# Performance work log

Measured on AMD Instinct MI355X. Metric: run time of the kernel, lower is better.

The kernel has to match this reference:

```python
import jax, jax.numpy as jnp
import numpy as np

B = 4096       # batch
D = 256        # num_features
H = 512        # proposal_hidden_units
K = 10         # mixture_components
C = 64         # context_units
L = 4          # proposal_residual_blocks
S = 10         # num_importance_samples (call default)
HEAD = 3 * K + C
LOG2PI = float(np.log(2.0 * np.pi))


def setup_inputs() -> dict:
    key = jax.random.key(0)
    ks = jax.random.split(key, 10)
    x = jax.random.normal(ks[0], (B, D), jnp.float32)
    observed_mask = (jax.random.uniform(ks[1], (B, D)) < 0.5).astype(jnp.float32)
    s_in = 1.0 / np.sqrt(2 * D)
    s_h = 1.0 / np.sqrt(H)
    W_in = (jax.random.normal(ks[2], (2 * D, H), jnp.float32) * s_in)
    b_in = jnp.zeros((H,), jnp.float32)
    W1 = jax.random.normal(ks[3], (L, H, H), jnp.float32) * s_h
    b1 = jnp.zeros((L, H), jnp.float32)
    W2 = jax.random.normal(ks[4], (L, H, H), jnp.float32) * s_h
    b2 = jnp.zeros((L, H), jnp.float32)
    W_fin = jax.random.normal(ks[5], (H, D * HEAD), jnp.float32) * s_h
    b_fin = jnp.zeros((D * HEAD,), jnp.float32)
    return {
        "x": x, "observed_mask": observed_mask,
        "W_in": W_in, "b_in": b_in,
        "W1": W1, "b1": b1, "W2": W2, "b2": b2,
        "W_fin": W_fin, "b_fin": b_fin,
        "num_importance_samples": S,
    }


def _proposal_params(x_o, observed_mask, W_in, b_in, W1, b1, W2, b2, W_fin, b_fin):
    # Residual MLP proposal network on [x_o, observed_mask].
    h = jnp.concatenate([x_o, observed_mask], axis=-1) @ W_in + b_in  # [B, H]
    for l in range(L):
        r = jax.nn.relu(h) @ W1[l] + b1[l]
        r = jax.nn.relu(r) @ W2[l] + b2[l]
        h = h + r
    out = (h @ W_fin + b_fin).reshape(h.shape[0], D, HEAD)  # [B, D, 3K+C]
    logits = out[..., :K]
    means = out[..., K:2 * K]
    scales = jax.nn.softplus(out[..., 2 * K:3 * K]) + 1e-3
    return logits, means, scales


def reference(x, observed_mask, W_in, b_in, W1, b1, W2, b2, W_fin, b_fin,
              num_importance_samples):
    query = 1.0 - observed_mask
    x_o = x * observed_mask
    x_u = x * query

    logits, means, scales = _proposal_params(
        x_o, observed_mask, W_in, b_in, W1, b1, W2, b2, W_fin, b_fin)

    # Per-feature mixture-of-Gaussians log-likelihood of x_u, masked by query.
    log_w = jax.nn.log_softmax(logits, axis=-1)               # [B, D, K]
    z = (x_u[..., None] - means) / scales
    comp_ll = -0.5 * z * z - jnp.log(scales) - 0.5 * LOG2PI   # [B, D, K]
    proposal_ll = jax.scipy.special.logsumexp(log_w + comp_ll, axis=-1) * query

    # Samples (stop_gradient in the original).
    skey = jax.random.key(1234)
    kc, kn = jax.random.split(skey)
    comp = jax.random.categorical(kc, logits, axis=-1,
                                  shape=(num_importance_samples,) + logits.shape[:2])  # [S, B, D]
    mu = jnp.take_along_axis(means[None], comp[..., None], axis=-1)[..., 0]    # [S, B, D]
    sg = jnp.take_along_axis(scales[None], comp[..., None], axis=-1)[..., 0]   # [S, B, D]
    eps = jax.random.normal(kn, comp.shape, jnp.float32)
    samples = mu + sg * eps                                   # [S, B, D]
    samples = jnp.transpose(samples, (1, 0, 2))               # [B, S, D]
    samples = jax.lax.stop_gradient(samples) * query[:, None, :]
    # call() multiplies by query twice (before and after selected_features block)
    proposal_samples = samples * query[:, None, :]

    proposal_mean = jnp.sum(jax.nn.softmax(logits, axis=-1) * means, axis=-1) * query
    proposal_mean = proposal_mean * query  # second masking, as in call()

    return proposal_ll, proposal_samples, proposal_mean
```

## Files before the change

### kernel.cpp

```cpp
#include <hip/hip_runtime.h>
#include <cstdint>

#define B 4096
#define D 256
#define H 512
#define K 10
#define NL 4
#define S 10
#define NOUT 30
#define HEADW 94
#define ND (B*D)
#define NLOG 2560
#define NMS  5120

typedef __bf16 bf16x8 __attribute__((ext_vector_type(8)));
typedef float  f32x16 __attribute__((ext_vector_type(16)));

__host__ __device__ inline void threefry2x32(uint32_t k0, uint32_t k1,
                                             uint32_t x0, uint32_t x1,
                                             uint32_t& o0, uint32_t& o1) {
  uint32_t ks2 = k0 ^ k1 ^ 0x1BD11BDAu;
#define TF_ROT(x, r) (((x) << (r)) | ((x) >> (32 - (r))))
#define TF_RND(r) { x0 += x1; x1 = TF_ROT(x1, r); x1 ^= x0; }
  x0 += k0; x1 += k1;
  TF_RND(13) TF_RND(15) TF_RND(26) TF_RND(6)
  x0 += k1; x1 += ks2 + 1u;
  TF_RND(17) TF_RND(29) TF_RND(16) TF_RND(24)
  x0 += ks2; x1 += k0 + 2u;
  TF_RND(13) TF_RND(15) TF_RND(26) TF_RND(6)
  x0 += k0; x1 += k1 + 3u;
  TF_RND(17) TF_RND(29) TF_RND(16) TF_RND(24)
  x0 += k1; x1 += ks2 + 4u;
  TF_RND(13) TF_RND(15) TF_RND(26) TF_RND(6)
  x0 += ks2; x1 += k0 + 5u;
  o0 = x0; o1 = x1;
#undef TF_RND
#undef TF_ROT
}

__device__ __forceinline__ uint32_t rb32(uint32_t k0, uint32_t k1, uint32_t idx) {
  uint32_t a, b;
  threefry2x32(k0, k1, 0u, idx, a, b);
  return a ^ b;
}

__device__ __forceinline__ float u01_from_bits(uint32_t bits) {
  return __uint_as_float((bits >> 9) | 0x3f800000u) - 1.0f;
}

__device__ __forceinline__ float erfinv_f32(float x) {
  float w = -log1pf(-x * x);
  float p;
  if (w < 5.0f) {
    w = w - 2.5f;
    p = 2.81022636e-08f;
    p = fmaf(p, w, 3.43273939e-07f);
    p = fmaf(p, w, -3.5233877e-06f);
    p = fmaf(p, w, -4.39150654e-06f);
    p = fmaf(p, w, 0.00021858087f);
    p = fmaf(p, w, -0.00125372503f);
    p = fmaf(p, w, -0.00417768164f);
    p = fmaf(p, w, 0.246640727f);
    p = fmaf(p, w, 1.50140941f);
  } else {
    w = sqrtf(w) - 3.0f;
    p = -0.000200214257f;
    p = fmaf(p, w, 0.000100950558f);
    p = fmaf(p, w, 0.00134934322f);
    p = fmaf(p, w, -0.00367342844f);
    p = fmaf(p, w, 0.00573950773f);
    p = fmaf(p, w, -0.0076224613f);
    p = fmaf(p, w, 0.00943887047f);
    p = fmaf(p, w, 1.00167406f);
    p = fmaf(p, w, 2.83297682f);
  }
  return p * x;
}

__device__ __forceinline__ unsigned short bf16_rne(float x) {
  uint32_t u = __float_as_uint(x);
  uint32_t r = u + 0x7fffu + ((u >> 16) & 1u);
  return (unsigned short)(r >> 16);
}

__device__ __forceinline__ void split2(float x, short& hi, short& lo) {
  unsigned short hb = bf16_rne(x);
  float hf = __uint_as_float((uint32_t)hb << 16);
  hi = (short)hb;
  lo = (short)bf16_rne(x - hf);
}

__device__ __forceinline__ void gload16(const void* g, void* l) {
  __builtin_amdgcn_global_load_lds(
      (const __attribute__((address_space(1))) void*)g,
      (__attribute__((address_space(3))) void*)l, 16, 0, 0);
}

template <int ROWS>
__device__ __forceinline__ void stage_region(const short* __restrict__ g,
                                             short* l, int wid, int lane) {
#pragma unroll
  for (int c = wid; c < ROWS / 16; c += 4) {
    const short* gp = g + (size_t)(c * 16 + (lane >> 2)) * 512 + (lane & 3) * 8;
    gload16(gp, l + c * 512);
  }
}

__global__ __launch_bounds__(256) void wgatherL(const float* __restrict__ Wf,
                                                float* __restrict__ wsgL) {
  int c = blockIdx.x * 256 + threadIdx.x;
  int k = blockIdx.y;
  int dd = c / K, j = c - dd * K;
  wsgL[(size_t)k * NLOG + c] = Wf[(size_t)k * (D * HEADW) + dd * HEADW + j];
}

__global__ __launch_bounds__(256) void wsplit_ms(const float* __restrict__ Wf,
                                                 short* __restrict__ whi,
                                                 short* __restrict__ wlo) {
  __shared__ float tile[32][33];
  int n0 = blockIdx.x * 32, k0 = blockIdx.y * 32;
  int tx = threadIdx.x & 31, ty = threadIdx.x >> 5;
#pragma unroll
  for (int r = 0; r < 4; ++r) {
    int k = k0 + ty + r * 8;
    int n = n0 + tx;
    int dd = n / 20, j = n - dd * 20;
    tile[ty + r * 8][tx] = Wf[(size_t)k * (D * HEADW) + dd * HEADW + 10 + j];
  }
  __syncthreads();
#pragma unroll
  for (int r = 0; r < 4; ++r) {
    int n = n0 + ty + r * 8;
    int k = k0 + tx;
    float v = tile[tx][ty + r * 8];
    short hb, lb;
    split2(v, hb, lb);
    whi[(size_t)n * 512 + k] = hb;
    wlo[(size_t)n * 512 + k] = lb;
  }
}

template <int RELU, int RES, int FP, int SPLIT>
__global__ __launch_bounds__(256) void gemm_trunk(const float* __restrict__ A,
                                                  const float* __restrict__ W,
                                                  const float* __restrict__ bias,
                                                  const float* res, float* C,
                                                  const float* __restrict__ xp,
                                                  const float* __restrict__ mp,
                                                  short* __restrict__ Ah,
                                                  short* __restrict__ Al) {
  __shared__ float As[64 * 68];
  __shared__ float Ws[64 * 64];
  const int tid = threadIdx.x;
  const int lane = tid & 63, wid = tid >> 6;
  const int tx = tid & 15, ty = tid >> 4;
  const int bm = blockIdx.y * 64, bn = blockIdx.x * 64;
  const int ls = tid & 15, lm = tid >> 4;

  float acc[4][4] = {};

  for (int k0 = 0; k0 < H; k0 += 64) {
#pragma unroll
    for (int c = wid; c < 16; c += 4) {
      gload16(W + (size_t)(k0 + c * 4 + (lane >> 4)) * H + bn + (lane & 15) * 4,
              Ws + c * 256 + lane * 4);
    }
#pragma unroll
    for (int r = 0; r < 4; ++r) {
      int m = lm + 16 * r;
      float4 f;
      if (FP) {
        int c = k0 + 4 * ls;
        const int brow = bm + m;
        if (c < D) {
          float4 xv = *(const float4*)(xp + (size_t)brow * D + c);
          float4 mv = *(const float4*)(mp + (size_t)brow * D + c);
          f.x = xv.x * mv.x; f.y = xv.y * mv.y;
          f.z = xv.z * mv.z; f.w = xv.w * mv.w;
        } else {
          f = *(const float4*)(mp + (size_t)brow * D + (c - D));
        }
      } else {
        f = *(const float4*)(A + (size_t)(bm + m) * H + k0 + 4 * ls);
      }
      if (RELU) {
        f.x = fmaxf(f.x, 0.0f); f.y = fmaxf(f.y, 0.0f);
        f.z = fmaxf(f.z, 0.0f); f.w = fmaxf(f.w, 0.0f);
      }
      As[(4 * ls + 0) * 68 + m] = f.x;
      As[(4 * ls + 1) * 68 + m] = f.y;
      As[(4 * ls + 2) * 68 + m] = f.z;
      As[(4 * ls + 3) * 68 + m] = f.w;
    }
    __syncthreads();
#pragma unroll
    for (int kk = 0; kk < 64; ++kk) {
      float4 a4 = *(const float4*)(As + kk * 68 + ty * 4);
      float4 b4 = *(const float4*)(Ws + kk * 64 + tx * 4);
      float a[4] = {a4.x, a4.y, a4.z, a4.w};
      float b[4] = {b4.x, b4.y, b4.z, b4.w};
#pragma unroll
      for (int i = 0; i < 4; ++i)
#pragma unroll
        for (int j = 0; j < 4; ++j) acc[i][j] = fmaf(a[i], b[j], acc[i][j]);
    }
    __syncthreads();
  }
#pragma unroll
  for (int i = 0; i < 4; ++i) {
    int row = bm + ty * 4 + i;
    float v[4];
#pragma unroll
    for (int j = 0; j < 4; ++j) {
      int col = bn + tx * 4 + j;
      v[j] = acc[i][j] + bias[col];
      if (RES) v[j] = res[(size_t)row * H + col] + v[j];
      C[(size_t)row * H + col] = v[j];
    }
    if (SPLIT) {
      short4 h4, l4;
      split2(v[0], h4.x, l4.x); split2(v[1], h4.y, l4.y);
      split2(v[2], h4.z, l4.z); split2(v[3], h4.w, l4.w);
      *(short4*)(Ah + (size_t)row * H + bn + tx * 4) = h4;
      *(short4*)(Al + (size_t)row * H + bn + tx * 4) = l4;
    }
  }
}

__global__ __launch_bounds__(256) void gemm_head(const float* __restrict__ A,
                                                 const float* __restrict__ Wg,
                                                 const short* __restrict__ Bh,
                                                 const short* __restrict__ Bl,
                                                 const short* __restrict__ Ah,
                                                 const short* __restrict__ Al,
                                                 const float* __restrict__ bf,
                                                 float* __restrict__ headL,
                                                 float* __restrict__ headMS) {
  __shared__ __align__(16) float smem[8448];
  const int tid = threadIdx.x;
  const int lane = tid & 63, wid = tid >> 6;
  const int bm = blockIdx.y * 128;

  if (blockIdx.x < 20) {
    float* As = smem;
    float* Ws = smem + 4352;
    const int tx = tid & 15, ty = tid >> 4;
    const int bn = blockIdx.x * 128;
    const int ls = tid & 7, lm = tid >> 3;

    float acc[8][8] = {};

    for (int k0 = 0; k0 < H; k0 += 32) {
#pragma unroll
      for (int c = wid; c < 16; c += 4) {
        gload16(Wg + (size_t)(k0 + c * 2 + (lane >> 5)) * NLOG + bn + (lane & 31) * 4,
                Ws + c * 256 + lane * 4);
      }
#pragma unroll
      for (int r = 0; r < 4; ++r) {
        int m = lm + 32 * r;
        float4 f = *(const float4*)(A + (size_t)(bm + m) * H + k0 + 4 * ls);
        As[(4 * ls + 0) * 136 + m] = f.x;
        As[(4 * ls + 1) * 136 + m] = f.y;
        As[(4 * ls + 2) * 136 + m] = f.z;
        As[(4 * ls + 3) * 136 + m] = f.w;
      }
      __syncthreads();
#pragma unroll
      for (int kk = 0; kk < 32; ++kk) {
        float a[8], b[8];
        *(float4*)(a + 0) = *(const float4*)(As + kk * 136 + ty * 8);
        *(float4*)(a + 4) = *(const float4*)(As + kk * 136 + ty * 8 + 4);
        *(float4*)(b + 0) = *(const float4*)(Ws + kk * 128 + tx * 8);
        *(float4*)(b + 4) = *(const float4*)(Ws + kk * 128 + tx * 8 + 4);
#pragma unroll
        for (int i = 0; i < 8; ++i)
#pragma unroll
          for (int j = 0; j < 8; ++j) acc[i][j] = fmaf(a[i], b[j], acc[i][j]);
      }
      __syncthreads();
    }
    float bias[8];
#pragma unroll
    for (int j = 0; j < 8; ++j) {
      int c = bn + tx * 8 + j;
      int dd = c / K, jj = c - dd * K;
      bias[j] = bf[dd * HEADW + jj];
    }
#pragma unroll
    for (int i = 0; i < 8; ++i) {
      int row = bm + ty * 8 + i;
      float4 v0, v1;
      v0.x = acc[i][0] + bias[0]; v0.y = acc[i][1] + bias[1];
      v0.z = acc[i][2] + bias[2]; v0.w = acc[i][3] + bias[3];
      v1.x = acc[i][4] + bias[4]; v1.y = acc[i][5] + bias[5];
      v1.z = acc[i][6] + bias[6]; v1.w = acc[i][7] + bias[7];
      float* dst = headL + (size_t)row * NLOG + bn + tx * 8;
      *(float4*)dst = v0;
      *(float4*)(dst + 4) = v1;
    }
  } else {
    short* lds = (short*)smem;
    const int wm = wid >> 1, wn = wid & 1;
    const int bn = (blockIdx.x - 20) * 128;

    short* ldsAh = lds;
    short* ldsAl = lds + 4096;
    short* ldsBh = lds + 8192;
    short* ldsBl = lds + 12288;

    const short* gBh = Bh + (size_t)bn * 512;
    const short* gBl = Bl + (size_t)bn * 512;
    const short* gAh = Ah + (size_t)bm * 512;
    const short* gAl = Al + (size_t)bm * 512;

    f32x16 acc[2][2];
#pragma unroll
    for (int mt = 0; mt < 2; ++mt)
#pragma unroll
      for (int nt = 0; nt < 2; ++nt)
#pragma unroll
        for (int i = 0; i < 16; ++i) acc[mt][nt][i] = 0.0f;

    for (int k0 = 0; k0 < 512; k0 += 32) {
      stage_region<128>(gBh + k0, ldsBh, wid, lane);
      stage_region<128>(gBl + k0, ldsBl, wid, lane);
      stage_region<128>(gAh + k0, ldsAh, wid, lane);
      stage_region<128>(gAl + k0, ldsAl, wid, lane);
      __syncthreads();
#pragma unroll
      for (int sub = 0; sub < 2; ++sub) {
        bf16x8 ah[2], al[2], bh[2], bl[2];
#pragma unroll
        for (int mt = 0; mt < 2; ++mt) {
          int r = wm * 64 + mt * 32 + (lane & 31);
          int off = r * 32 + sub * 16 + (lane >> 5) * 8;
          ah[mt] = *(const bf16x8*)(ldsAh + off);
          al[mt] = *(const bf16x8*)(ldsAl + off);
        }
#pragma unroll
        for (int nt = 0; nt < 2; ++nt) {
          int r = wn * 64 + nt * 32 + (lane & 31);
          int off = r * 32 + sub * 16 + (lane >> 5) * 8;
          bh[nt] = *(const bf16x8*)(ldsBh + off);
          bl[nt] = *(const bf16x8*)(ldsBl + off);
        }
#pragma unroll
        for (int mt = 0; mt < 2; ++mt)
#pragma unroll
          for (int nt = 0; nt < 2; ++nt) {
            acc[mt][nt] = __builtin_amdgcn_mfma_f32_32x32x16_bf16(ah[mt], bh[nt], acc[mt][nt], 0, 0, 0);
            acc[mt][nt] = __builtin_amdgcn_mfma_f32_32x32x16_bf16(ah[mt], bl[nt], acc[mt][nt], 0, 0, 0);
            acc[mt][nt] = __builtin_amdgcn_mfma_f32_32x32x16_bf16(al[mt], bh[nt], acc[mt][nt], 0, 0, 0);
          }
      }
      __syncthreads();
    }

#pragma unroll
    for (int mt = 0; mt < 2; ++mt)
#pragma unroll
      for (int nt = 0; nt < 2; ++nt) {
        int col = bn + wn * 64 + nt * 32 + (lane & 31);
        int rbase = bm + wm * 64 + mt * 32 + 4 * (lane >> 5);
        int dd = col / 20, j = col - dd * 20;
#pragma unroll
        for (int reg = 0; reg < 16; ++reg) {
          int row = rbase + (reg & 3) + 8 * (reg >> 2);
          float v = acc[mt][nt][reg] + bf[dd * HEADW + 10 + j];
          if (j >= 10) v = (fmaxf(v, 0.0f) + log1pf(expf(-fabsf(v)))) + 0.001f;
          headMS[(size_t)row * NMS + col] = v;
        }
      }
  }
}

__global__ __launch_bounds__(256) void compact_zero(const float* __restrict__ mask,
                                                    float* __restrict__ out_ll,
                                                    float* __restrict__ out_s,
                                                    float* __restrict__ out_mean,
                                                    int* __restrict__ list,
                                                    int* __restrict__ counter) {
  int idx = blockIdx.x * 256 + threadIdx.x;
  if (idx >= ND) return;
  if (mask[idx] != 0.0f) {
    int b = idx >> 8, d = idx & (D - 1);
    out_ll[idx] = 0.0f;
    out_mean[idx] = 0.0f;
#pragma unroll
    for (int s = 0; s < S; ++s) out_s[((size_t)b * S + s) * D + d] = 0.0f;
  } else {
    int pos = atomicAdd(counter, 1);
    list[pos] = idx;
  }
}

__global__ __launch_bounds__(256) void fused_tail(const float* __restrict__ headL,
                                                  const float* __restrict__ headMS,
                                                  const float* __restrict__ x,
                                                  const float* __restrict__ mask,
                                                  const int* __restrict__ list,
                                                  const int* __restrict__ counter,
                                                  float* __restrict__ out_ll,
                                                  float* __restrict__ out_s,
                                                  float* __restrict__ out_mean,
                                                  uint32_t kc0, uint32_t kc1,
                                                  uint32_t kn0, uint32_t kn1) {
  int i = blockIdx.x * 256 + threadIdx.x;
  if (i >= *counter) return;
  int idx = list[i];
  int b = idx >> 8, d = idx & (D - 1);
  const float* hpL = headL + (size_t)idx * K;
  const float* hpM = headMS + (size_t)idx * (2 * K);
  float lg[K], mn[K], sc[K];
#pragma unroll
  for (int k = 0; k < K; ++k) { lg[k] = hpL[k]; mn[k] = hpM[k]; sc[k] = hpM[K + k]; }
  float q = 1.0f - mask[idx];
  float xu = x[idx] * q;
  float m = lg[0];
#pragma unroll
  for (int k = 1; k < K; ++k) m = fmaxf(m, lg[k]);
  float e[K];
  float sum = 0.0f;
#pragma unroll
  for (int k = 0; k < K; ++k) { e[k] = expf(lg[k] - m); sum += e[k]; }
  float lse = logf(sum);
  float a[K];
  float amax = -3.402823466e38f;
#pragma unroll
  for (int k = 0; k < K; ++k) {
    float z = (xu - mn[k]) / sc[k];
    float cll = -0.5f * z * z - logf(sc[k]) - 0.9189385332046727f;
    float lw = (lg[k] - m) - lse;
    a[k] = lw + cll;
    amax = fmaxf(amax, a[k]);
  }
  float s2 = 0.0f;
#pragma unroll
  for (int k = 0; k < K; ++k) s2 += expf(a[k] - amax);
  out_ll[idx] = (logf(s2) + amax) * q;
  float pm = 0.0f;
#pragma unroll
  for (int k = 0; k < K; ++k) pm += (e[k] / sum) * mn[k];
  out_mean[idx] = pm * q;
  float inv_e[K];
#pragma unroll
  for (int k = 0; k < K; ++k) inv_e[k] = 1.0f / e[k];
  for (int s = 0; s < S; ++s) {
    uint32_t t32 = (uint32_t)s * (uint32_t)ND + (uint32_t)idx;
    uint32_t base = t32 * (uint32_t)K;
    int best = 0;
    float rbest = 3.402823466e38f;
#pragma unroll
    for (int k = 0; k < K; ++k) {
      uint32_t bits = rb32(kc0, kc1, base + (uint32_t)k);
      float u = u01_from_bits(bits);
      float wv = -__log2f(u);
      float r = wv * inv_e[k];
      if (r < rbest) { rbest = r; best = k; }
    }
    uint32_t ebits = rb32(kn0, kn1, t32);
    float f = u01_from_bits(ebits);
    float r2 = f * 2.0f + (-0.99999994f);
    r2 = fmaxf(r2, -0.99999994f);
    float eps = 1.4142135623730951f * erfinv_f32(r2);
    out_s[((size_t)b * S + s) * D + d] = (mn[best] + sc[best] * eps) * q;
  }
}

extern "C" void kernel_launch(void* const* d_in, const int* in_sizes, int n_in,
                              void* d_out, int out_size, void* d_ws, size_t ws_size,
                              hipStream_t stream) {
  const float* x    = (const float*)d_in[0];
  const float* mask = (const float*)d_in[1];
  const float* W_in = (const float*)d_in[2];
  const float* b_in = (const float*)d_in[3];
  const float* W1   = (const float*)d_in[4];
  const float* b1   = (const float*)d_in[5];
  const float* W2   = (const float*)d_in[6];
  const float* b2   = (const float*)d_in[7];
  const float* Wf   = (const float*)d_in[8];
  const float* bf   = (const float*)d_in[9];

  char* w = (char*)d_ws;
  float* headL  = (float*)w;
  float* headMS = (float*)(w + 41943040);
  float* t      = headL;
  float* h      = (float*)(w + 125829120);
  float* wsgL   = (float*)(w + 134217728);
  int*   list   = (int*)(w + 134217728);
  short* wms_h  = (short*)(w + 139460608);
  short* wms_l  = (short*)(w + 144703488);
  int*   counter = (int*)(w + 149946368);

  float* out_ll   = (float*)d_out;
  float* out_s    = out_ll + (size_t)ND;
  float* out_mean = out_s + (size_t)ND * S;

  short* Ah = (short*)out_s;
  short* Al = Ah + (size_t)B * H;

  wgatherL<<<dim3(NLOG / 256, 512), 256, 0, stream>>>(Wf, wsgL);
  wsplit_ms<<<dim3(NMS / 32, 512 / 32), 256, 0, stream>>>(Wf, wms_h, wms_l);

  dim3 gtr(H / 64, B / 64);
  gemm_trunk<0, 0, 1, 0><<<gtr, 256, 0, stream>>>(nullptr, W_in, b_in, nullptr,
                                                  h, x, mask, nullptr, nullptr);
  for (int l = 0; l < NL - 1; ++l) {
    gemm_trunk<1, 0, 0, 0><<<gtr, 256, 0, stream>>>(h, W1 + (size_t)l * H * H,
                                                    b1 + (size_t)l * H, nullptr,
                                                    t, nullptr, nullptr,
                                                    nullptr, nullptr);
    gemm_trunk<1, 1, 0, 0><<<gtr, 256, 0, stream>>>(t, W2 + (size_t)l * H * H,
                                                    b2 + (size_t)l * H, h, h,
                                                    nullptr, nullptr,
                                                    nullptr, nullptr);
  }
  gemm_trunk<1, 0, 0, 0><<<gtr, 256, 0, stream>>>(h, W1 + (size_t)3 * H * H,
                                                  b1 + (size_t)3 * H, nullptr,
                                                  t, nullptr, nullptr,
                                                  nullptr, nullptr);
  gemm_trunk<1, 1, 0, 1><<<gtr, 256, 0, stream>>>(t, W2 + (size_t)3 * H * H,
                                                  b2 + (size_t)3 * H, h, h,
                                                  nullptr, nullptr, Ah, Al);

  gemm_head<<<dim3(60, B / 128), 256, 0, stream>>>(h, wsgL, wms_h, wms_l,
                                                   Ah, Al, bf, headL, headMS);

  hipMemsetAsync(counter, 0, 4, stream);
  compact_zero<<<ND / 256, 256, 0, stream>>>(mask, out_ll, out_s, out_mean,
                                             list, counter);

  uint32_t kc0, kc1, kn0, kn1;
  threefry2x32(0u, 1234u, 0u, 0u, kc0, kc1);
  threefry2x32(0u, 1234u, 0u, 1u, kn0, kn1);
  fused_tail<<<ND / 256, 256, 0, stream>>>(headL, headMS, x, mask, list, counter,
                                           out_ll, out_s, out_mean,
                                           kc0, kc1, kn0, kn1);
}
```

Before: 1.130 ms.

## Fuse head weight gather and split kernels into first trunk GEMM launch

Removes the separate wgatherL and wsplit_ms launches. Their work now runs as extra blocks (blockIdx.x >= 8) inside the first trunk GEMM grid. The weight preprocessing overlaps with the input GEMM and two kernel launches go away. The grid grows to 128x64 blocks, and the extra blocks return early, which may change scheduling of the GEMM blocks.

After: 1.216 ms. 1.08x slower.

```diff
diff --git a/kernel.cpp b/kernel.cpp
--- a/kernel.cpp
+++ b/kernel.cpp
@@ -106,41 +106,7 @@
   }
 }
 
-__global__ __launch_bounds__(256) void wgatherL(const float* __restrict__ Wf,
-                                                float* __restrict__ wsgL) {
-  int c = blockIdx.x * 256 + threadIdx.x;
-  int k = blockIdx.y;
-  int dd = c / K, j = c - dd * K;
-  wsgL[(size_t)k * NLOG + c] = Wf[(size_t)k * (D * HEADW) + dd * HEADW + j];
-}
-
-__global__ __launch_bounds__(256) void wsplit_ms(const float* __restrict__ Wf,
-                                                 short* __restrict__ whi,
-                                                 short* __restrict__ wlo) {
-  __shared__ float tile[32][33];
-  int n0 = blockIdx.x * 32, k0 = blockIdx.y * 32;
-  int tx = threadIdx.x & 31, ty = threadIdx.x >> 5;
-#pragma unroll
-  for (int r = 0; r < 4; ++r) {
-    int k = k0 + ty + r * 8;
-    int n = n0 + tx;
-    int dd = n / 20, j = n - dd * 20;
-    tile[ty + r * 8][tx] = Wf[(size_t)k * (D * HEADW) + dd * HEADW + 10 + j];
-  }
-  __syncthreads();
-#pragma unroll
-  for (int r = 0; r < 4; ++r) {
-    int n = n0 + ty + r * 8;
-    int k = k0 + tx;
-    float v = tile[tx][ty + r * 8];
-    short hb, lb;
-    split2(v, hb, lb);
-    whi[(size_t)n * 512 + k] = hb;
-    wlo[(size_t)n * 512 + k] = lb;
-  }
-}
-
-template <int RELU, int RES, int FP, int SPLIT>
+template <int RELU, int RES, int FP, int SPLIT, int WP>
 __global__ __launch_bounds__(256) void gemm_trunk(const float* __restrict__ A,
                                                   const float* __restrict__ W,
                                                   const float* __restrict__ bias,
@@ -148,10 +114,49 @@
                                                   const float* __restrict__ xp,
                                                   const float* __restrict__ mp,
                                                   short* __restrict__ Ah,
-                                                  short* __restrict__ Al) {
+                                                  short* __restrict__ Al,
+                                                  const float* __restrict__ Wf,
+                                                  float* __restrict__ wsgL,
+                                                  short* __restrict__ whi,
+                                                  short* __restrict__ wlo) {
   __shared__ float As[64 * 68];
   __shared__ float Ws[64 * 64];
   const int tid = threadIdx.x;
+
+  if (WP && blockIdx.x >= 8) {
+    const int id = (blockIdx.x - 8) * 64 + blockIdx.y;
+    if (id < 5120) {
+      int c = (id % 10) * 256 + tid;
+      int k = id / 10;
+      int dd = c / K, j = c - dd * K;
+      wsgL[(size_t)k * NLOG + c] = Wf[(size_t)k * (D * HEADW) + dd * HEADW + j];
+    } else {
+      float (*tile)[33] = (float(*)[33])As;
+      int b2 = id - 5120;
+      int n0 = (b2 % 160) * 32, k0 = (b2 / 160) * 32;
+      int tx = tid & 31, ty = tid >> 5;
+#pragma unroll
+      for (int r = 0; r < 4; ++r) {
+        int k = k0 + ty + r * 8;
+        int n = n0 + tx;
+        int dd = n / 20, j = n - dd * 20;
+        tile[ty + r * 8][tx] = Wf[(size_t)k * (D * HEADW) + dd * HEADW + 10 + j];
+      }
+      __syncthreads();
+#pragma unroll
+      for (int r = 0; r < 4; ++r) {
+        int n = n0 + ty + r * 8;
+        int k = k0 + tx;
+        float v = tile[tx][ty + r * 8];
+        short hb, lb;
+        split2(v, hb, lb);
+        whi[(size_t)n * 512 + k] = hb;
+        wlo[(size_t)n * 512 + k] = lb;
+      }
+    }
+    return;
+  }
+
   const int lane = tid & 63, wid = tid >> 6;
   const int tx = tid & 15, ty = tid >> 4;
   const int bm = blockIdx.y * 64, bn = blockIdx.x * 64;
@@ -500,29 +505,25 @@
   short* Ah = (short*)out_s;
   short* Al = Ah + (size_t)B * H;
 
-  wgatherL<<<dim3(NLOG / 256, 512), 256, 0, stream>>>(Wf, wsgL);
-  wsplit_ms<<<dim3(NMS / 32, 512 / 32), 256, 0, stream>>>(Wf, wms_h, wms_l);
+  gemm_trunk<0, 0, 1, 0, 1><<<dim3(128, 64), 256, 0, stream>>>(
+      nullptr, W_in, b_in, nullptr, h, x, mask, nullptr, nullptr,
+      Wf, wsgL, wms_h, wms_l);
 
   dim3 gtr(H / 64, B / 64);
-  gemm_trunk<0, 0, 1, 0><<<gtr, 256, 0, stream>>>(nullptr, W_in, b_in, nullptr,
-                                                  h, x, mask, nullptr, nullptr);
   for (int l = 0; l < NL - 1; ++l) {
-    gemm_trunk<1, 0, 0, 0><<<gtr, 256, 0, stream>>>(h, W1 + (size_t)l * H * H,
-                                                    b1 + (size_t)l * H, nullptr,
-                                                    t, nullptr, nullptr,
-                                                    nullptr, nullptr);
-    gemm_trunk<1, 1, 0, 0><<<gtr, 256, 0, stream>>>(t, W2 + (size_t)l * H * H,
-                                                    b2 + (size_t)l * H, h, h,
-                                                    nullptr, nullptr,
-                                                    nullptr, nullptr);
-  }
-  gemm_trunk<1, 0, 0, 0><<<gtr, 256, 0, stream>>>(h, W1 + (size_t)3 * H * H,
-                                                  b1 + (size_t)3 * H, nullptr,
-                                                  t, nullptr, nullptr,
-                                                  nullptr, nullptr);
-  gemm_trunk<1, 1, 0, 1><<<gtr, 256, 0, stream>>>(t, W2 + (size_t)3 * H * H,
-                                                  b2 + (size_t)3 * H, h, h,
-                                                  nullptr, nullptr, Ah, Al);
+    gemm_trunk<1, 0, 0, 0, 0><<<gtr, 256, 0, stream>>>(
+        h, W1 + (size_t)l * H * H, b1 + (size_t)l * H, nullptr, t,
+        nullptr, nullptr, nullptr, nullptr, nullptr, nullptr, nullptr, nullptr);
+    gemm_trunk<1, 1, 0, 0, 0><<<gtr, 256, 0, stream>>>(
+        t, W2 + (size_t)l * H * H, b2 + (size_t)l * H, h, h,
+        nullptr, nullptr, nullptr, nullptr, nullptr, nullptr, nullptr, nullptr);
+  }
+  gemm_trunk<1, 0, 0, 0, 0><<<gtr, 256, 0, stream>>>(
+      h, W1 + (size_t)3 * H * H, b1 + (size_t)3 * H, nullptr, t,
+      nullptr, nullptr, nullptr, nullptr, nullptr, nullptr, nullptr, nullptr);
+  gemm_trunk<1, 1, 0, 1, 0><<<gtr, 256, 0, stream>>>(
+      t, W2 + (size_t)3 * H * H, b2 + (size_t)3 * H, h, h,
+      nullptr, nullptr, Ah, Al, nullptr, nullptr, nullptr, nullptr);
 
   gemm_head<<<dim3(60, B / 128), 256, 0, stream>>>(h, wsgL, wms_h, wms_l,
                                                    Ah, Al, bf, headL, headMS);
```
